# Optimization experiments

Measured on AMD Instinct MI355X. Metric: run time of the kernel, lower is better.

The kernel has to match this reference:

```python
import jax, jax.numpy as jnp
import numpy as np
import math

B, T, C, H = 4, 2048, 1024, 16
DH = C // H  # 64

def setup_inputs() -> dict:
    key = jax.random.key(0)
    k1, k2, k3 = jax.random.split(key, 3)
    x = jax.random.normal(k1, (B, T, C), dtype=jnp.float32)
    # standard RoPE angle table: [T, DH/2]
    inv_freq = 1.0 / (10000.0 ** (jnp.arange(0, DH, 2, dtype=jnp.float32) / DH))
    ang = jnp.arange(T, dtype=jnp.float32)[:, None] * inv_freq[None, :]
    cos = jnp.cos(ang)
    sin = jnp.sin(ang)
    Wqkv = jax.random.normal(k2, (3 * C, C), dtype=jnp.float32) * (C ** -0.5)
    Wo = jax.random.normal(k3, (C, C), dtype=jnp.float32) * (C ** -0.5)
    return {"x": x, "cos": cos, "sin": sin, "Wqkv": Wqkv, "Wo": Wo}

def apply_rotary(x, cos, sin):
    # x: [B,H,T,DH]; cos/sin: [T, DH/2] broadcast over B,H
    x1, x2 = x[..., ::2], x[..., 1::2]
    xr = jnp.stack([x1 * cos - x2 * sin, x1 * sin + x2 * cos], axis=-1)
    return xr.reshape(x.shape)

def reference(x, cos, sin, Wqkv, Wo):
    Bz, Tz, Cz = x.shape
    qkv = x @ Wqkv.T  # [B,T,3C]
    q, k, v = jnp.split(qkv, 3, axis=-1)
    def heads(t):
        return t.reshape(Bz, Tz, H, DH).transpose(0, 2, 1, 3)  # [B,H,T,DH]
    q, k, v = heads(q), heads(k), heads(v)
    q = apply_rotary(q, cos, sin)
    k = apply_rotary(k, cos, sin)
    attn = jnp.einsum('bhqd,bhkd->bhqk', q, k) / math.sqrt(DH)
    causal = jnp.tril(jnp.ones((Tz, Tz), dtype=bool))
    attn = jnp.where(causal, attn, jnp.float32(-jnp.inf))
    attn = jax.nn.softmax(attn, axis=-1)
    y = jnp.einsum('bhqk,bhkd->bhqd', attn, v)
    y = y.transpose(0, 2, 1, 3).reshape(Bz, Tz, Cz)
    return y @ Wo.T
```

## Files before the change

### kernel.cpp

```cpp
#include <hip/hip_runtime.h>
#include <math.h>

#define Bz 4
#define Tz 2048
#define Cz 1024
#define Hz 16
#define DHz 64
#define Mz (Bz*Tz)

typedef __attribute__((ext_vector_type(8))) short short8;
typedef __attribute__((ext_vector_type(4))) float f32x4;
typedef __attribute__((ext_vector_type(4))) float flt4;

__device__ inline unsigned short f2bf(float f){
  union { float f; unsigned int u; } x; x.f = f;
  unsigned int r = x.u + 0x7fffu + ((x.u >> 16) & 1u);
  return (unsigned short)(r >> 16);
}
__device__ inline float bf2f(unsigned short b){
  union { unsigned int u; float f; } x; x.u = ((unsigned int)b) << 16; return x.f;
}
__device__ inline unsigned int packbf2(float a, float b){
  union { float f; unsigned int u; } x, y; x.f = a; y.f = b;
  return (x.u >> 16) | (y.u & 0xffff0000u);
}

__device__ inline void gload_lds16(const unsigned short* g, char* l){
  __builtin_amdgcn_global_load_lds((const __attribute__((address_space(1))) unsigned int*)g,
                                   (__attribute__((address_space(3))) unsigned int*)l,
                                   16, 0, 0);
}

__global__ __launch_bounds__(256) void cvt_bf16(const float* __restrict__ src,
                                                unsigned short* __restrict__ dst, int n){
  int i = (blockIdx.x * 256 + threadIdx.x) * 4;
  if (i + 3 < n){
    flt4 v = *(const flt4*)(src + i);
    unsigned short o0 = f2bf(v.x), o1 = f2bf(v.y), o2 = f2bf(v.z), o3 = f2bf(v.w);
    unsigned long long pack = (unsigned long long)o0 | ((unsigned long long)o1 << 16)
                            | ((unsigned long long)o2 << 32) | ((unsigned long long)o3 << 48);
    *(unsigned long long*)(dst + i) = pack;
  }
}

template<int EPI>
__global__ __launch_bounds__(256)
void gemm_bt(const unsigned short* __restrict__ A, const unsigned short* __restrict__ Bw,
             const int K,
             unsigned short* __restrict__ qd, unsigned short* __restrict__ kd,
             unsigned short* __restrict__ vd, float* __restrict__ outf)
{
  __shared__ __align__(16) char lds[32768];
  char* At = lds;
  char* Bt = lds + 16384;

  const int tid  = threadIdx.x;
  const int lane = tid & 63, wid = tid >> 6;
  const int l16  = lane & 15, lg = lane >> 4;
  const int wr   = wid >> 1, wc = wid & 1;
  const int m0   = blockIdx.y * 128, n0 = blockIdx.x * 128;

  f32x4 acc[4][4] = {};
  const int nk = K >> 6;

  for (int kt = 0; kt < nk; ++kt){
    const unsigned short* As = A  + (size_t)m0 * K + kt * 64;
    const unsigned short* Bs = Bw + (size_t)n0 * K + kt * 64;
    #pragma unroll
    for (int it = 0; it < 4; ++it){
      int id  = it * 256 + tid;
      int row = id >> 3, c = id & 7;
      int sc  = c ^ (row & 7);
      char* dA = At + (it * 256 + wid * 64) * 16;
      char* dB = Bt + (it * 256 + wid * 64) * 16;
      gload_lds16(As + (size_t)row * K + sc * 8, dA);
      gload_lds16(Bs + (size_t)row * K + sc * 8, dB);
    }
    __syncthreads();

    #pragma unroll
    for (int ks = 0; ks < 2; ++ks){
      short8 af[4], bf[4];
      #pragma unroll
      for (int mt = 0; mt < 4; ++mt){
        int row = wr * 64 + mt * 16 + l16;
        af[mt] = *(const short8*)(At + row * 128 + (((ks * 4 + lg) ^ (row & 7)) << 4));
      }
      #pragma unroll
      for (int nt = 0; nt < 4; ++nt){
        int row = wc * 64 + nt * 16 + l16;
        bf[nt] = *(const short8*)(Bt + row * 128 + (((ks * 4 + lg) ^ (row & 7)) << 4));
      }
      #pragma unroll
      for (int mt = 0; mt < 4; ++mt)
        #pragma unroll
        for (int nt = 0; nt < 4; ++nt)
          acc[mt][nt] = __builtin_amdgcn_mfma_f32_16x16x32_bf16(af[mt], bf[nt], acc[mt][nt], 0, 0, 0);
    }
    __syncthreads();
  }

  #pragma unroll
  for (int mt = 0; mt < 4; ++mt){
    #pragma unroll
    for (int nt = 0; nt < 4; ++nt){
      #pragma unroll
      for (int i = 0; i < 4; ++i){
        int m = m0 + wr * 64 + mt * 16 + lg * 4 + i;
        int n = n0 + wc * 64 + nt * 16 + l16;
        float val = acc[mt][nt][i];
        if (EPI == 0){
          int part = n >> 10, c = n & 1023;
          int h = c >> 6,  d = c & 63;
          int b = m >> 11, t = m & 2047;
          unsigned short* dst = (part == 0) ? qd : ((part == 1) ? kd : vd);
          dst[(((size_t)(b * Hz + h)) * Tz + t) * DHz + d] = f2bf(val);
        } else {
          outf[(size_t)m * 1024 + n] = val;
        }
      }
    }
  }
}

__global__ __launch_bounds__(256) void rope_kernel(unsigned short* __restrict__ qh,
                                                   unsigned short* __restrict__ kh,
                                                   const float* __restrict__ cosb,
                                                   const float* __restrict__ sinb){
  unsigned int idx = blockIdx.x * 256 + threadIdx.x;
  int i   = idx & 31;
  int row = (idx >> 5) & 131071;
  int buf = idx >> 22;
  unsigned short* p = (buf ? kh : qh) + (size_t)row * DHz + 2 * i;
  int t = row & (Tz - 1);
  float c = cosb[t * 32 + i], s = sinb[t * 32 + i];
  unsigned int pr = *(const unsigned int*)p;
  float x1 = bf2f((unsigned short)(pr & 0xffff));
  float x2 = bf2f((unsigned short)(pr >> 16));
  float r1 = x1 * c - x2 * s;
  float r2 = x1 * s + x2 * c;
  if (!buf){
    const float qs = 0.125f * 1.4426950408889634f;
    r1 *= qs; r2 *= qs;
  }
  *(unsigned int*)p = (unsigned int)f2bf(r1) | ((unsigned int)f2bf(r2) << 16);
}

__global__ __launch_bounds__(256)
void transpose_v(const unsigned short* __restrict__ src, unsigned short* __restrict__ dst){
  __shared__ __align__(16) unsigned short tl[64 * 72];
  const int tid = threadIdx.x;
  const int bh = blockIdx.x >> 5, tt = blockIdx.x & 31;
  const unsigned short* s = src + (((size_t)bh * Tz) + tt * 64) * DHz;
  {
    int r = tid >> 2, c0 = (tid & 3) * 16;
    short8 v0 = *(const short8*)(s + r * DHz + c0);
    short8 v1 = *(const short8*)(s + r * DHz + c0 + 8);
    *(short8*)(tl + r * 72 + c0) = v0;
    *(short8*)(tl + r * 72 + c0 + 8) = v1;
  }
  __syncthreads();
  const int d = tid & 63, w = tid >> 6;
  short8 a, b;
  #pragma unroll
  for (int j = 0; j < 8; ++j) a[j] = (short)tl[(w * 16 + j) * 72 + d];
  #pragma unroll
  for (int j = 0; j < 8; ++j) b[j] = (short)tl[(w * 16 + 8 + j) * 72 + d];
  unsigned short* o = dst + ((size_t)bh * DHz + d) * Tz + tt * 64 + w * 16;
  *(short8*)(o)     = a;
  *(short8*)(o + 8) = b;
}

__global__ __launch_bounds__(256)
void attn_fwd(const unsigned short* __restrict__ qh, const unsigned short* __restrict__ kh,
              const unsigned short* __restrict__ vt, unsigned short* __restrict__ y)
{
  __shared__ __align__(16) char lds[2*8192 + 2*8192 + 4*2304];
  const int tid  = threadIdx.x;
  const int lane = tid & 63, wid = tid >> 6;
  const int l16  = lane & 15, lg = lane >> 4;
  const int bh   = blockIdx.x;
  const int qt   = 31 - blockIdx.y;

  const size_t base = (size_t)bh * Tz * DHz;
  const unsigned short* qb = qh + base;
  const unsigned short* kb = kh + base;
  const unsigned short* vb = vt + base;

  const int qrow = qt * 64 + wid * 16 + l16;
  short8 qf[2];
  qf[0] = *(const short8*)(qb + (size_t)qrow * DHz + 0  + lg * 8);
  qf[1] = *(const short8*)(qb + (size_t)qrow * DHz + 32 + lg * 8);

  const int srow = tid >> 3;
  const int scol = (tid & 7) ^ (srow & 7);
  const int kOff = srow * DHz + scol * 8;
  const size_t vOff = (size_t)srow * Tz + scol * 8;
  char* const dst0 = (char*)lds + (wid * 64) * 16;

  auto STAGE = [&](int kt, int c){
    const unsigned short* Ks = kb + (size_t)kt * 64 * DHz;
    const unsigned short* Vs = vb + kt * 64;
    char* KD = (char*)lds + c * 8192;
    char* VD = (char*)lds + 16384 + c * 8192;
    #pragma unroll
    for (int it = 0; it < 2; ++it){
      gload_lds16(Ks + kOff + it * 32 * DHz, KD + (it * 256 + wid * 64) * 16);
      gload_lds16(Vs + vOff + (size_t)it * 32 * Tz, VD + (it * 256 + wid * 64) * 16);
    }
  };

  f32x4 o[4] = {};
  float m_r = -INFINITY, l_r = 0.f;
  unsigned short* Pw = (unsigned short*)(lds + 32768 + wid * 2304);

  int cur = 0;
  STAGE(0, 0);
  __syncthreads();

  for (int kt = 0; kt <= qt; ++kt){
    if (kt < qt) STAGE(kt + 1, cur ^ 1);

    char* KL = (char*)lds + cur * 8192;
    char* VL = (char*)lds + 16384 + cur * 8192;

    f32x4 s[4] = {};
    #pragma unroll
    for (int ks = 0; ks < 2; ++ks)
      #pragma unroll
      for (int nt = 0; nt < 4; ++nt){
        int row = nt * 16 + l16;
        short8 kf = *(const short8*)(KL + row * 128 + (((ks * 4 + lg) ^ (row & 7)) << 4));
        s[nt] = __builtin_amdgcn_mfma_f32_16x16x32_bf16(kf, qf[ks], s[nt], 0, 0, 0);
      }

    if (kt == qt){
      #pragma unroll
      for (int nt = 0; nt < 4; ++nt)
        #pragma unroll
        for (int r = 0; r < 4; ++r){
          int kv = kt * 64 + nt * 16 + lg * 4 + r;
          if (kv > qrow) s[nt][r] = -INFINITY;
        }
    }

    float mx = fmaxf(fmaxf(fmaxf(s[0][0], s[0][1]), fmaxf(s[0][2], s[0][3])),
               fmaxf(fmaxf(fmaxf(s[1][0], s[1][1]), fmaxf(s[1][2], s[1][3])),
               fmaxf(fmaxf(fmaxf(s[2][0], s[2][1]), fmaxf(s[2][2], s[2][3])),
                     fmaxf(fmaxf(s[3][0], s[3][1]), fmaxf(s[3][2], s[3][3])))));
    mx = fmaxf(mx, __shfl_xor(mx, 16));
    mx = fmaxf(mx, __shfl_xor(mx, 32));

    if (!__all(mx - m_r <= 8.0f)){
      float mn = fmaxf(m_r, mx);
      float al = __builtin_amdgcn_exp2f(m_r - mn);
      #pragma unroll
      for (int i = 0; i < 4; ++i){
        float ali = __shfl(al, lg * 4 + i);
        o[0][i] *= ali; o[1][i] *= ali; o[2][i] *= ali; o[3][i] *= ali;
      }
      l_r *= al; m_r = mn;
    }

    float p[4][4]; float rs = 0.f;
    #pragma unroll
    for (int nt = 0; nt < 4; ++nt)
      #pragma unroll
      for (int r = 0; r < 4; ++r){
        float pv = __builtin_amdgcn_exp2f(s[nt][r] - m_r);
        p[nt][r] = pv; rs += pv;
      }
    rs += __shfl_xor(rs, 16);
    rs += __shfl_xor(rs, 32);
    l_r += rs;

    #pragma unroll
    for (int nt = 0; nt < 4; ++nt){
      unsigned long long w64 = (unsigned long long)packbf2(p[nt][0], p[nt][1])
                             | ((unsigned long long)packbf2(p[nt][2], p[nt][3]) << 32);
      *(unsigned long long*)(Pw + l16 * 72 + nt * 16 + lg * 4) = w64;
    }

    #pragma unroll
    for (int ks = 0; ks < 2; ++ks){
      short8 pa = *(const short8*)((const char*)Pw + (l16 * 72 + ks * 32 + lg * 8) * 2);
      #pragma unroll
      for (int nt = 0; nt < 4; ++nt){
        int row = nt * 16 + l16;
        short8 vf = *(const short8*)(VL + row * 128 + (((ks * 4 + lg) ^ (row & 7)) << 4));
        o[nt] = __builtin_amdgcn_mfma_f32_16x16x32_bf16(pa, vf, o[nt], 0, 0, 0);
      }
    }

    __syncthreads();
    cur ^= 1;
  }

  const int b = bh >> 4, h = bh & 15;
  unsigned short* yb = y + ((size_t)b * Tz + qt * 64 + wid * 16) * Cz + h * 64;
  #pragma unroll
  for (int i = 0; i < 4; ++i){
    float inv = 1.f / __shfl(l_r, lg * 4 + i);
    int qr = lg * 4 + i;
    #pragma unroll
    for (int nt = 0; nt < 4; ++nt)
      yb[(size_t)qr * Cz + nt * 16 + l16] = f2bf(o[nt][i] * inv);
  }
}

extern "C" void kernel_launch(void* const* d_in, const int* in_sizes, int n_in,
                              void* d_out, int out_size, void* d_ws, size_t ws_size,
                              hipStream_t stream)
{
  const float* x    = (const float*)d_in[0];
  const float* cosb = (const float*)d_in[1];
  const float* sinb = (const float*)d_in[2];
  const float* Wqkv = (const float*)d_in[3];
  const float* Wo   = (const float*)d_in[4];
  float* out = (float*)d_out;

  char* ws = (char*)d_ws;
  unsigned short* xb    = (unsigned short*)(ws);
  unsigned short* vtb   = (unsigned short*)(ws);
  unsigned short* wqkvb = (unsigned short*)(ws + 16777216);
  unsigned short* wob   = (unsigned short*)(ws + 23068672);
  unsigned short* qhb   = (unsigned short*)(ws + 25165824);
  unsigned short* khb   = (unsigned short*)(ws + 41943040);
  unsigned short* vhb   = (unsigned short*)(ws + 58720256);
  unsigned short* ybuf  = vhb;

  cvt_bf16<<<8192, 256, 0, stream>>>(x,    xb,    Mz * Cz);
  cvt_bf16<<<3072, 256, 0, stream>>>(Wqkv, wqkvb, 3 * Cz * Cz);
  cvt_bf16<<<1024, 256, 0, stream>>>(Wo,   wob,   Cz * Cz);

  dim3 g1(24, 64);
  gemm_bt<0><<<g1, 256, 0, stream>>>(xb, wqkvb, Cz, qhb, khb, vhb, nullptr);

  rope_kernel<<<32768, 256, 0, stream>>>(qhb, khb, cosb, sinb);

  transpose_v<<<2048, 256, 0, stream>>>(vhb, vtb);

  dim3 g2(64, 32);
  attn_fwd<<<g2, 256, 0, stream>>>(qhb, khb, vtb, ybuf);

  dim3 g3(8, 64);
  gemm_bt<1><<<g3, 256, 0, stream>>>(ybuf, wob, Cz, nullptr, nullptr, nullptr, out);
}
```

Before: 286.8 us.

## Fuse conversions, write V transposed from GEMM, vectorize RoPE, restructure attention softmax

The three fp32-to-bf16 conversion launches become one kernel. The QKV GEMM epilogue now writes V directly in transposed layout, which removes the separate transpose kernel. RoPE processes eight elements per thread with vector loads. In attention, the MFMA operand order is swapped so each lane holds a whole row, and the row sum is computed with an MFMA against a ones vector, which removes the shuffles. It also adds s_setprio around the MFMA blocks, uses perm-based bf16 packing and writes the output in vectors, at the cost of extra MFMA work for the sum and strided V stores in the GEMM.

```diff
diff --git a/kernel.cpp b/kernel.cpp
--- a/kernel.cpp
+++ b/kernel.cpp
@@ -11,6 +11,7 @@
 typedef __attribute__((ext_vector_type(8))) short short8;
 typedef __attribute__((ext_vector_type(4))) float f32x4;
 typedef __attribute__((ext_vector_type(4))) float flt4;
+typedef unsigned long long u64;
 
 __device__ inline unsigned short f2bf(float f){
   union { float f; unsigned int u; } x; x.f = f;
@@ -20,9 +21,9 @@
 __device__ inline float bf2f(unsigned short b){
   union { unsigned int u; float f; } x; x.u = ((unsigned int)b) << 16; return x.f;
 }
-__device__ inline unsigned int packbf2(float a, float b){
-  union { float f; unsigned int u; } x, y; x.f = a; y.f = b;
-  return (x.u >> 16) | (y.u & 0xffff0000u);
+__device__ inline unsigned int packbf2(float lo, float hi){
+  union { float f; unsigned int u; } a, b; a.f = lo; b.f = hi;
+  return __builtin_amdgcn_perm(b.u, a.u, 0x07060302u);
 }
 
 __device__ inline void gload_lds16(const unsigned short* g, char* l){
@@ -31,16 +32,24 @@
                                    16, 0, 0);
 }
 
-__global__ __launch_bounds__(256) void cvt_bf16(const float* __restrict__ src,
-                                                unsigned short* __restrict__ dst, int n){
+#define NXE 8388608
+#define NW1 3145728
+#define NW2 1048576
+__global__ __launch_bounds__(256) void cvt_all(const float* __restrict__ x,
+                                               const float* __restrict__ wq,
+                                               const float* __restrict__ wo,
+                                               unsigned short* __restrict__ xb,
+                                               unsigned short* __restrict__ wqb,
+                                               unsigned short* __restrict__ wob){
   int i = (blockIdx.x * 256 + threadIdx.x) * 4;
-  if (i + 3 < n){
-    flt4 v = *(const flt4*)(src + i);
-    unsigned short o0 = f2bf(v.x), o1 = f2bf(v.y), o2 = f2bf(v.z), o3 = f2bf(v.w);
-    unsigned long long pack = (unsigned long long)o0 | ((unsigned long long)o1 << 16)
-                            | ((unsigned long long)o2 << 32) | ((unsigned long long)o3 << 48);
-    *(unsigned long long*)(dst + i) = pack;
-  }
+  const float* s; unsigned short* d;
+  if (i < NXE){ s = x + i; d = xb + i; }
+  else if (i < NXE + NW1){ s = wq + (i - NXE); d = wqb + (i - NXE); }
+  else { s = wo + (i - NXE - NW1); d = wob + (i - NXE - NW1); }
+  flt4 v = *(const flt4*)s;
+  u64 pack = (u64)f2bf(v.x) | ((u64)f2bf(v.y) << 16)
+           | ((u64)f2bf(v.z) << 32) | ((u64)f2bf(v.w) << 48);
+  *(u64*)d = pack;
 }
 
 template<int EPI>
@@ -100,25 +109,46 @@
     __syncthreads();
   }
 
-  #pragma unroll
-  for (int mt = 0; mt < 4; ++mt){
-    #pragma unroll
-    for (int nt = 0; nt < 4; ++nt){
-      #pragma unroll
-      for (int i = 0; i < 4; ++i){
-        int m = m0 + wr * 64 + mt * 16 + lg * 4 + i;
-        int n = n0 + wc * 64 + nt * 16 + l16;
-        float val = acc[mt][nt][i];
-        if (EPI == 0){
-          int part = n >> 10, c = n & 1023;
-          int h = c >> 6,  d = c & 63;
+  if (EPI == 1){
+    #pragma unroll
+    for (int mt = 0; mt < 4; ++mt)
+      #pragma unroll
+      for (int nt = 0; nt < 4; ++nt)
+        #pragma unroll
+        for (int i = 0; i < 4; ++i){
+          int m = m0 + wr * 64 + mt * 16 + lg * 4 + i;
+          int n = n0 + wc * 64 + nt * 16 + l16;
+          outf[(size_t)m * 1024 + n] = acc[mt][nt][i];
+        }
+  } else {
+    const int part = n0 >> 10;
+    if (part < 2){
+      unsigned short* dst = part ? kd : qd;
+      #pragma unroll
+      for (int mt = 0; mt < 4; ++mt)
+        #pragma unroll
+        for (int nt = 0; nt < 4; ++nt)
+          #pragma unroll
+          for (int i = 0; i < 4; ++i){
+            int m = m0 + wr * 64 + mt * 16 + lg * 4 + i;
+            int n = (n0 & 1023) + wc * 64 + nt * 16 + l16;
+            int h = n >> 6, d = n & 63;
+            int b = m >> 11, t = m & 2047;
+            dst[(((size_t)(b * Hz + h)) * Tz + t) * DHz + d] = f2bf(acc[mt][nt][i]);
+          }
+    } else {
+      #pragma unroll
+      for (int mt = 0; mt < 4; ++mt)
+        #pragma unroll
+        for (int nt = 0; nt < 4; ++nt){
+          int m = m0 + wr * 64 + mt * 16 + lg * 4;
+          int n = (n0 & 1023) + wc * 64 + nt * 16 + l16;
+          int h = n >> 6, d = n & 63;
           int b = m >> 11, t = m & 2047;
-          unsigned short* dst = (part == 0) ? qd : ((part == 1) ? kd : vd);
-          dst[(((size_t)(b * Hz + h)) * Tz + t) * DHz + d] = f2bf(val);
-        } else {
-          outf[(size_t)m * 1024 + n] = val;
+          u64 w = (u64)f2bf(acc[mt][nt][0]) | ((u64)f2bf(acc[mt][nt][1]) << 16)
+                | ((u64)f2bf(acc[mt][nt][2]) << 32) | ((u64)f2bf(acc[mt][nt][3]) << 48);
+          *(u64*)(vd + (((size_t)(b * Hz + h)) * DHz + d) * Tz + t) = w;
         }
-      }
     }
   }
 }
@@ -128,47 +158,27 @@
                                                    const float* __restrict__ cosb,
                                                    const float* __restrict__ sinb){
   unsigned int idx = blockIdx.x * 256 + threadIdx.x;
-  int i   = idx & 31;
-  int row = (idx >> 5) & 131071;
-  int buf = idx >> 22;
-  unsigned short* p = (buf ? kh : qh) + (size_t)row * DHz + 2 * i;
+  int quad = idx & 7;
+  int row  = (idx >> 3) & 131071;
+  int buf  = idx >> 20;
+  unsigned short* p = (buf ? kh : qh) + (size_t)row * DHz + quad * 8;
   int t = row & (Tz - 1);
-  float c = cosb[t * 32 + i], s = sinb[t * 32 + i];
-  unsigned int pr = *(const unsigned int*)p;
-  float x1 = bf2f((unsigned short)(pr & 0xffff));
-  float x2 = bf2f((unsigned short)(pr >> 16));
-  float r1 = x1 * c - x2 * s;
-  float r2 = x1 * s + x2 * c;
-  if (!buf){
-    const float qs = 0.125f * 1.4426950408889634f;
-    r1 *= qs; r2 *= qs;
-  }
-  *(unsigned int*)p = (unsigned int)f2bf(r1) | ((unsigned int)f2bf(r2) << 16);
-}
-
-__global__ __launch_bounds__(256)
-void transpose_v(const unsigned short* __restrict__ src, unsigned short* __restrict__ dst){
-  __shared__ __align__(16) unsigned short tl[64 * 72];
-  const int tid = threadIdx.x;
-  const int bh = blockIdx.x >> 5, tt = blockIdx.x & 31;
-  const unsigned short* s = src + (((size_t)bh * Tz) + tt * 64) * DHz;
-  {
-    int r = tid >> 2, c0 = (tid & 3) * 16;
-    short8 v0 = *(const short8*)(s + r * DHz + c0);
-    short8 v1 = *(const short8*)(s + r * DHz + c0 + 8);
-    *(short8*)(tl + r * 72 + c0) = v0;
-    *(short8*)(tl + r * 72 + c0 + 8) = v1;
-  }
-  __syncthreads();
-  const int d = tid & 63, w = tid >> 6;
-  short8 a, b;
+  flt4 c = *(const flt4*)(cosb + t * 32 + quad * 4);
+  flt4 s = *(const flt4*)(sinb + t * 32 + quad * 4);
+  short8 v = *(const short8*)p;
+  const float qs = 0.125f * 1.4426950408889634f;
+  float sc = buf ? 1.0f : qs;
+  short8 o;
   #pragma unroll
-  for (int j = 0; j < 8; ++j) a[j] = (short)tl[(w * 16 + j) * 72 + d];
-  #pragma unroll
-  for (int j = 0; j < 8; ++j) b[j] = (short)tl[(w * 16 + 8 + j) * 72 + d];
-  unsigned short* o = dst + ((size_t)bh * DHz + d) * Tz + tt * 64 + w * 16;
-  *(short8*)(o)     = a;
-  *(short8*)(o + 8) = b;
+  for (int j = 0; j < 4; ++j){
+    float x1 = bf2f((unsigned short)v[2*j]);
+    float x2 = bf2f((unsigned short)v[2*j+1]);
+    float r1 = (x1 * c[j] - x2 * s[j]) * sc;
+    float r2 = (x1 * s[j] + x2 * c[j]) * sc;
+    o[2*j]   = (short)f2bf(r1);
+    o[2*j+1] = (short)f2bf(r2);
+  }
+  *(short8*)p = o;
 }
 
 __global__ __launch_bounds__(256)
@@ -192,11 +202,17 @@
   qf[0] = *(const short8*)(qb + (size_t)qrow * DHz + 0  + lg * 8);
   qf[1] = *(const short8*)(qb + (size_t)qrow * DHz + 32 + lg * 8);
 
+  const int x07 = l16 & 7;
+  const int fo0 = l16 * 128 + (((0 + lg) ^ x07) << 4);
+  const int fo1 = l16 * 128 + (((4 + lg) ^ x07) << 4);
+  char* const Pb  = (char*)lds + 32768 + wid * 2304;
+  const int pwo = (l16 * 72 + lg * 4) * 2;
+  const int pro = (l16 * 72 + lg * 8) * 2;
+
   const int srow = tid >> 3;
   const int scol = (tid & 7) ^ (srow & 7);
   const int kOff = srow * DHz + scol * 8;
   const size_t vOff = (size_t)srow * Tz + scol * 8;
-  char* const dst0 = (char*)lds + (wid * 64) * 16;
 
   auto STAGE = [&](int kt, int c){
     const unsigned short* Ks = kb + (size_t)kt * 64 * DHz;
@@ -205,14 +221,18 @@
     char* VD = (char*)lds + 16384 + c * 8192;
     #pragma unroll
     for (int it = 0; it < 2; ++it){
-      gload_lds16(Ks + kOff + it * 32 * DHz, KD + (it * 256 + wid * 64) * 16);
-      gload_lds16(Vs + vOff + (size_t)it * 32 * Tz, VD + (it * 256 + wid * 64) * 16);
+      gload_lds16(Ks + kOff + it * 32 * DHz, KD + it * 4096 + wid * 1024);
+      gload_lds16(Vs + vOff + (size_t)it * 32 * Tz, VD + it * 4096 + wid * 1024);
     }
   };
 
+  short8 ones;
+  #pragma unroll
+  for (int j = 0; j < 8; ++j) ones[j] = (short)0x3F80;
+
   f32x4 o[4] = {};
-  float m_r = -INFINITY, l_r = 0.f;
-  unsigned short* Pw = (unsigned short*)(lds + 32768 + wid * 2304);
+  f32x4 lsum = {};
+  float m_r = -INFINITY;
 
   int cur = 0;
   STAGE(0, 0);
@@ -221,18 +241,22 @@
   for (int kt = 0; kt <= qt; ++kt){
     if (kt < qt) STAGE(kt + 1, cur ^ 1);
 
-    char* KL = (char*)lds + cur * 8192;
-    char* VL = (char*)lds + 16384 + cur * 8192;
+    const char* KL = (const char*)lds + cur * 8192;
+    const char* VL = (const char*)lds + 16384 + cur * 8192;
 
     f32x4 s[4] = {};
-    #pragma unroll
-    for (int ks = 0; ks < 2; ++ks)
-      #pragma unroll
-      for (int nt = 0; nt < 4; ++nt){
-        int row = nt * 16 + l16;
-        short8 kf = *(const short8*)(KL + row * 128 + (((ks * 4 + lg) ^ (row & 7)) << 4));
-        s[nt] = __builtin_amdgcn_mfma_f32_16x16x32_bf16(kf, qf[ks], s[nt], 0, 0, 0);
-      }
+    __builtin_amdgcn_s_setprio(1);
+    #pragma unroll
+    for (int nt = 0; nt < 4; ++nt){
+      short8 kf = *(const short8*)(KL + fo0 + nt * 2048);
+      s[nt] = __builtin_amdgcn_mfma_f32_16x16x32_bf16(kf, qf[0], s[nt], 0, 0, 0);
+    }
+    #pragma unroll
+    for (int nt = 0; nt < 4; ++nt){
+      short8 kf = *(const short8*)(KL + fo1 + nt * 2048);
+      s[nt] = __builtin_amdgcn_mfma_f32_16x16x32_bf16(kf, qf[1], s[nt], 0, 0, 0);
+    }
+    __builtin_amdgcn_s_setprio(0);
 
     if (kt == qt){
       #pragma unroll
@@ -244,10 +268,10 @@
         }
     }
 
-    float mx = fmaxf(fmaxf(fmaxf(s[0][0], s[0][1]), fmaxf(s[0][2], s[0][3])),
-               fmaxf(fmaxf(fmaxf(s[1][0], s[1][1]), fmaxf(s[1][2], s[1][3])),
-               fmaxf(fmaxf(fmaxf(s[2][0], s[2][1]), fmaxf(s[2][2], s[2][3])),
-                     fmaxf(fmaxf(s[3][0], s[3][1]), fmaxf(s[3][2], s[3][3])))));
+    float mx = fmaxf(fmaxf(fmaxf(fmaxf(s[0][0], s[0][1]), fmaxf(s[0][2], s[0][3])),
+                           fmaxf(fmaxf(s[1][0], s[1][1]), fmaxf(s[1][2], s[1][3]))),
+                     fmaxf(fmaxf(fmaxf(s[2][0], s[2][1]), fmaxf(s[2][2], s[2][3])),
+                           fmaxf(fmaxf(s[3][0], s[3][1]), fmaxf(s[3][2], s[3][3]))));
     mx = fmaxf(mx, __shfl_xor(mx, 16));
     mx = fmaxf(mx, __shfl_xor(mx, 32));
 
@@ -255,56 +279,51 @@
       float mn = fmaxf(m_r, mx);
       float al = __builtin_amdgcn_exp2f(m_r - mn);
       #pragma unroll
-      for (int i = 0; i < 4; ++i){
-        float ali = __shfl(al, lg * 4 + i);
-        o[0][i] *= ali; o[1][i] *= ali; o[2][i] *= ali; o[3][i] *= ali;
+      for (int nt = 0; nt < 4; ++nt)
+        #pragma unroll
+        for (int i = 0; i < 4; ++i) o[nt][i] *= al;
+      #pragma unroll
+      for (int i = 0; i < 4; ++i) lsum[i] *= al;
+      m_r = mn;
+    }
+
+    #pragma unroll
+    for (int nt = 0; nt < 4; ++nt){
+      float p0 = __builtin_amdgcn_exp2f(s[nt][0] - m_r);
+      float p1 = __builtin_amdgcn_exp2f(s[nt][1] - m_r);
+      float p2 = __builtin_amdgcn_exp2f(s[nt][2] - m_r);
+      float p3 = __builtin_amdgcn_exp2f(s[nt][3] - m_r);
+      u64 w = (u64)packbf2(p0, p1) | ((u64)packbf2(p2, p3) << 32);
+      *(u64*)(Pb + pwo + nt * 32) = w;
+    }
+
+    __builtin_amdgcn_s_setprio(1);
+    #pragma unroll
+    for (int ks = 0; ks < 2; ++ks){
+      short8 pa = *(const short8*)(Pb + pro + ks * 64);
+      lsum = __builtin_amdgcn_mfma_f32_16x16x32_bf16(ones, pa, lsum, 0, 0, 0);
+      const int fo = ks ? fo1 : fo0;
+      #pragma unroll
+      for (int nt = 0; nt < 4; ++nt){
+        short8 vf = *(const short8*)(VL + fo + nt * 2048);
+        o[nt] = __builtin_amdgcn_mfma_f32_16x16x32_bf16(vf, pa, o[nt], 0, 0, 0);
       }
-      l_r *= al; m_r = mn;
-    }
-
-    float p[4][4]; float rs = 0.f;
-    #pragma unroll
-    for (int nt = 0; nt < 4; ++nt)
-      #pragma unroll
-      for (int r = 0; r < 4; ++r){
-        float pv = __builtin_amdgcn_exp2f(s[nt][r] - m_r);
-        p[nt][r] = pv; rs += pv;
-      }
-    rs += __shfl_xor(rs, 16);
-    rs += __shfl_xor(rs, 32);
-    l_r += rs;
-
-    #pragma unroll
-    for (int nt = 0; nt < 4; ++nt){
-      unsigned long long w64 = (unsigned long long)packbf2(p[nt][0], p[nt][1])
-                             | ((unsigned long long)packbf2(p[nt][2], p[nt][3]) << 32);
-      *(unsigned long long*)(Pw + l16 * 72 + nt * 16 + lg * 4) = w64;
-    }
-
-    #pragma unroll
-    for (int ks = 0; ks < 2; ++ks){
-      short8 pa = *(const short8*)((const char*)Pw + (l16 * 72 + ks * 32 + lg * 8) * 2);
-      #pragma unroll
-      for (int nt = 0; nt < 4; ++nt){
-        int row = nt * 16 + l16;
-        short8 vf = *(const short8*)(VL + row * 128 + (((ks * 4 + lg) ^ (row & 7)) << 4));
-        o[nt] = __builtin_amdgcn_mfma_f32_16x16x32_bf16(pa, vf, o[nt], 0, 0, 0);
-      }
-    }
+    }
+    __builtin_amdgcn_s_setprio(0);
 
     __syncthreads();
     cur ^= 1;
   }
 
   const int b = bh >> 4, h = bh & 15;
-  unsigned short* yb = y + ((size_t)b * Tz + qt * 64 + wid * 16) * Cz + h * 64;
+  const int row = qt * 64 + wid * 16 + l16;
+  unsigned short* yb = y + ((size_t)b * Tz + row) * Cz + h * 64 + lg * 4;
+  float inv = 1.f / lsum[0];
   #pragma unroll
-  for (int i = 0; i < 4; ++i){
-    float inv = 1.f / __shfl(l_r, lg * 4 + i);
-    int qr = lg * 4 + i;
-    #pragma unroll
-    for (int nt = 0; nt < 4; ++nt)
-      yb[(size_t)qr * Cz + nt * 16 + l16] = f2bf(o[nt][i] * inv);
+  for (int nt = 0; nt < 4; ++nt){
+    u64 w = (u64)f2bf(o[nt][0] * inv) | ((u64)f2bf(o[nt][1] * inv) << 16)
+          | ((u64)f2bf(o[nt][2] * inv) << 32) | ((u64)f2bf(o[nt][3] * inv) << 48);
+    *(u64*)(yb + nt * 16) = w;
   }
 }
 
@@ -321,24 +340,19 @@
 
   char* ws = (char*)d_ws;
   unsigned short* xb    = (unsigned short*)(ws);
-  unsigned short* vtb   = (unsigned short*)(ws);
+  unsigned short* ybuf  = xb;
   unsigned short* wqkvb = (unsigned short*)(ws + 16777216);
   unsigned short* wob   = (unsigned short*)(ws + 23068672);
   unsigned short* qhb   = (unsigned short*)(ws + 25165824);
   unsigned short* khb   = (unsigned short*)(ws + 41943040);
-  unsigned short* vhb   = (unsigned short*)(ws + 58720256);
-  unsigned short* ybuf  = vhb;
-
-  cvt_bf16<<<8192, 256, 0, stream>>>(x,    xb,    Mz * Cz);
-  cvt_bf16<<<3072, 256, 0, stream>>>(Wqkv, wqkvb, 3 * Cz * Cz);
-  cvt_bf16<<<1024, 256, 0, stream>>>(Wo,   wob,   Cz * Cz);
+  unsigned short* vtb   = (unsigned short*)(ws + 58720256);
+
+  cvt_all<<<12288, 256, 0, stream>>>(x, Wqkv, Wo, xb, wqkvb, wob);
 
   dim3 g1(24, 64);
-  gemm_bt<0><<<g1, 256, 0, stream>>>(xb, wqkvb, Cz, qhb, khb, vhb, nullptr);
-
-  rope_kernel<<<32768, 256, 0, stream>>>(qhb, khb, cosb, sinb);
-
-  transpose_v<<<2048, 256, 0, stream>>>(vhb, vtb);
+  gemm_bt<0><<<g1, 256, 0, stream>>>(xb, wqkvb, Cz, qhb, khb, vtb, nullptr);
+
+  rope_kernel<<<8192, 256, 0, stream>>>(qhb, khb, cosb, sinb);
 
   dim3 g2(64, 32);
   attn_fwd<<<g2, 256, 0, stream>>>(qhb, khb, vtb, ybuf);
```

Result: faster. 266.2 us (-7.2%).
